# Optimization experiments

Measured on AMD Instinct MI355X. Metric: run time of the kernel, lower is better.

Reference implementation:

```python
import jax, jax.numpy as jnp
import numpy as np

NUM_HEADS = 16
EPS = 1e-5
BLOCK = 16  # score_mod: q_idx // 16 == kv_idx % 16


def _ln(x, eps=EPS):
    # LayerNorm, elementwise_affine=False
    m = jnp.mean(x, axis=-1, keepdims=True)
    v = jnp.mean((x - m) ** 2, axis=-1, keepdims=True)
    return (x - m) * jax.lax.rsqrt(v + eps)


def setup_inputs() -> dict:
    key = jax.random.key(0)
    ks = jax.random.split(key, 5)
    N, D = 2048, 2048
    w = 0.02
    return {
        "x": jax.random.normal(ks[0], (N, D), jnp.float32),
        "Wq": jax.random.normal(ks[1], (D, D), jnp.float32) * w,
        "Wk": jax.random.normal(ks[2], (D, D), jnp.float32) * w,
        "Wv": jax.random.normal(ks[3], (D, D), jnp.float32) * w,
        "Wo": jax.random.normal(ks[4], (D, D), jnp.float32) * w,
    }


def reference(x, Wq, Wk, Wv, Wo):
    N, D = x.shape
    H = NUM_HEADS
    DH = D // H
    x_in = x
    xn = _ln(x)
    # per-head q/k layernorm, cast to attention dtype (bfloat16)
    q = _ln((xn @ Wq).reshape(N, H, DH)).astype(jnp.bfloat16)
    k = _ln((xn @ Wk).reshape(N, H, DH)).astype(jnp.bfloat16)
    v = (xn @ Wv).reshape(N, H, DH)  # stays fp32 (original applies no cast to vs)
    scale = 1.0 / np.sqrt(DH)
    # dense scores then sparsity mask, as flex_attention with score_mod does
    scores = jnp.einsum("nhd,mhd->hnm", q, k, preferred_element_type=jnp.float32) * scale
    qi = jnp.arange(N)
    mask = (qi[:, None] // BLOCK) == (qi[None, :] % BLOCK)  # [N, N]
    s = jnp.where(mask[None, :, :], scores, -jnp.inf)
    # safe softmax: rows with no allowed keys (q_idx >= 256) produce zeros
    mx = jnp.max(s, axis=-1, keepdims=True)
    e = jnp.exp(s - jnp.where(jnp.isfinite(mx), mx, 0.0))
    denom = jnp.sum(e, axis=-1, keepdims=True)
    attn = e / jnp.maximum(denom, 1e-30)
    o = jnp.einsum("hnm,mhd->nhd", attn, v)  # [N, H, DH]
    out = o.reshape(N, D) @ Wo
    return out + x_in
```

## Files before the change

kernel.cpp:

```cpp
#include <hip/hip_runtime.h>

typedef unsigned short u16;
typedef __attribute__((ext_vector_type(8))) short short8;
typedef __attribute__((ext_vector_type(4))) float f32x4;

#define D 2048
#define EPS 1e-5f

__device__ __forceinline__ u16 f2bf(float f) {
  unsigned u = __float_as_uint(f);
  u += 0x7fffu + ((u >> 16) & 1u);
  return (u16)(u >> 16);
}

__device__ __forceinline__ void async16(const void* g, void* l) {
  __builtin_amdgcn_global_load_lds(
      (const __attribute__((address_space(1))) void*)g,
      (__attribute__((address_space(3))) void*)l, 16, 0, 0);
}

__global__ __launch_bounds__(256) void prep(const float* __restrict__ x,
                                            const float* __restrict__ Wq,
                                            const float* __restrict__ Wk,
                                            const float* __restrict__ Wv,
                                            const float* __restrict__ Wo,
                                            u16* __restrict__ xn,
                                            float* __restrict__ out,
                                            u16* __restrict__ WqT, u16* __restrict__ WkT,
                                            u16* __restrict__ WvT, u16* __restrict__ WoT) {
  int bid = blockIdx.x;
  int t = threadIdx.x;
  if (bid < 2048) {
    const float* xr = x + (size_t)bid * D;
    float4 v[2];
    float s = 0.f, sq = 0.f;
#pragma unroll
    for (int i = 0; i < 2; i++) {
      v[i] = *(const float4*)(xr + i * 1024 + t * 4);
      s += v[i].x + v[i].y + v[i].z + v[i].w;
      sq += v[i].x * v[i].x + v[i].y * v[i].y + v[i].z * v[i].z + v[i].w * v[i].w;
    }
#pragma unroll
    for (int m = 32; m >= 1; m >>= 1) { s += __shfl_xor(s, m); sq += __shfl_xor(sq, m); }
    __shared__ float ps[4], pq[4];
    int w = t >> 6, lane = t & 63;
    if (lane == 0) { ps[w] = s; pq[w] = sq; }
    __syncthreads();
    s = ps[0] + ps[1] + ps[2] + ps[3];
    sq = pq[0] + pq[1] + pq[2] + pq[3];
    float mean = s * (1.f / D);
    float var = sq * (1.f / D) - mean * mean;
    float rs = rsqrtf(var + EPS);
    float* outr = out + (size_t)bid * D;
    u16* xnr = xn + (size_t)bid * D;
#pragma unroll
    for (int i = 0; i < 2; i++) {
      *(float4*)(outr + i * 1024 + t * 4) = v[i];
      ushort4 o;
      o.x = f2bf((v[i].x - mean) * rs);
      o.y = f2bf((v[i].y - mean) * rs);
      o.z = f2bf((v[i].z - mean) * rs);
      o.w = f2bf((v[i].w - mean) * rs);
      *(ushort4*)(xnr + i * 1024 + t * 4) = o;
    }
  } else {
    int tb = bid - 2048;
    int wsel = tb >> 10;
    int tt = tb & 1023;
    const float* src; u16* dst;
    switch (wsel) {
      case 0: src = Wq; dst = WqT; break;
      case 1: src = Wk; dst = WkT; break;
      case 2: src = Wv; dst = WvT; break;
      default: src = Wo; dst = WoT; break;
    }
    int i0 = (tt >> 5) * 64, j0 = (tt & 31) * 64;
    __shared__ u16 tile[64 * 66];
#pragma unroll
    for (int r = 0; r < 4; r++) {
      int idx = r * 256 + t;
      int row = idx >> 4, c4 = idx & 15;
      float4 v = *(const float4*)(src + (size_t)(i0 + row) * D + j0 + c4 * 4);
      tile[row * 66 + c4 * 4 + 0] = f2bf(v.x);
      tile[row * 66 + c4 * 4 + 1] = f2bf(v.y);
      tile[row * 66 + c4 * 4 + 2] = f2bf(v.z);
      tile[row * 66 + c4 * 4 + 3] = f2bf(v.w);
    }
    __syncthreads();
#pragma unroll
    for (int r = 0; r < 4; r++) {
      int idx = r * 256 + t;
      int row = idx >> 4, c4 = idx & 15;
      ushort4 o;
      o.x = tile[(c4 * 4 + 0) * 66 + row];
      o.y = tile[(c4 * 4 + 1) * 66 + row];
      o.z = tile[(c4 * 4 + 2) * 66 + row];
      o.w = tile[(c4 * 4 + 3) * 66 + row];
      *(ushort4*)(dst + (size_t)(j0 + row) * D + i0 + c4 * 4) = o;
    }
  }
}

__device__ __forceinline__ void gemm_tile(const u16* __restrict__ A,
                                          const u16* __restrict__ Bt,
                                          bool permB, int m0, int n0,
                                          int kbeg, int kend,
                                          u16* As, u16* Bs, f32x4 acc[4][4]) {
  int tid = threadIdx.x, wid = tid >> 6, lane = tid & 63;
  int q4 = lane >> 4, m16 = lane & 15;
  int wm = wid >> 1, wn = wid & 1;
  for (int kb = kbeg; kb < kend; kb += 64) {
#pragma unroll
    for (int p = 0; p < 4; p++) {
      int idx = p * 256 + tid;
      int r = idx >> 3, sl = idx & 7;
      int gc = sl ^ (r & 7);
      async16(A + (size_t)(m0 + r) * D + kb + gc * 8, As + (size_t)(p * 256 + wid * 64) * 8);
      int rb = n0 + r;
      int gr = permB ? ((rb & 127) * 16 + (rb >> 7)) : rb;
      async16(Bt + (size_t)gr * D + kb + gc * 8, Bs + (size_t)(p * 256 + wid * 64) * 8);
    }
    __syncthreads();
#pragma unroll
    for (int ks = 0; ks < 2; ks++) {
      short8 af[4], bf[4];
      int c = ks * 4 + q4;
#pragma unroll
      for (int i = 0; i < 4; i++) {
        int ra = wm * 64 + i * 16 + m16;
        af[i] = *(const short8*)(As + ra * 64 + (c ^ (ra & 7)) * 8);
        int rb = wn * 64 + i * 16 + m16;
        bf[i] = *(const short8*)(Bs + rb * 64 + (c ^ (rb & 7)) * 8);
      }
#pragma unroll
      for (int i = 0; i < 4; i++)
#pragma unroll
        for (int j = 0; j < 4; j++)
          acc[i][j] = __builtin_amdgcn_mfma_f32_16x16x32_bf16(af[i], bf[j], acc[i][j], 0, 0, 0);
    }
    __syncthreads();
  }
}

__global__ __launch_bounds__(256, 3) void gemm_mega(const u16* __restrict__ xn,
                                                    const u16* __restrict__ WkT,
                                                    const u16* __restrict__ WqT,
                                                    const u16* __restrict__ WvT,
                                                    u16* __restrict__ K3,
                                                    u16* __restrict__ Q3,
                                                    u16* __restrict__ V3) {
  __shared__ u16 smem[2 * 128 * 64];
  u16* As = smem;
  u16* Bs = smem + 8192;
  int bid = blockIdx.x;
  int sel = (bid < 256) ? 0 : (bid < 512) ? 2 : 1;
  int z = (sel == 1) ? bid - 512 : (bid & 255);
  int m0 = (z >> 4) * 128, n0 = (z & 15) * 128;
  const u16* A = (sel == 2) ? WvT : xn;
  const u16* Bt = (sel == 0) ? WkT : (sel == 1) ? WqT : xn;
  f32x4 acc[4][4];
#pragma unroll
  for (int i = 0; i < 4; i++)
#pragma unroll
    for (int j = 0; j < 4; j++)
#pragma unroll
      for (int r = 0; r < 4; r++) acc[i][j][r] = 0.f;
  gemm_tile(A, Bt, sel == 2, m0, n0, 0, D, As, Bs, acc);

  int tid = threadIdx.x, wid = tid >> 6, lane = tid & 63;
  int q4 = lane >> 4, m16 = lane & 15;
  int wm = wid >> 1, wn = wid & 1;
  if (sel == 2) {
    int h = m0 >> 7, b = n0 >> 7;
#pragma unroll
    for (int i = 0; i < 4; i++)
#pragma unroll
      for (int j = 0; j < 4; j++)
#pragma unroll
        for (int r = 0; r < 4; r++) {
          int dhl = wm * 64 + i * 16 + q4 * 4 + r;
          int key = wn * 64 + j * 16 + m16;
          V3[((size_t)(h * 16 + b) * 128 + dhl) * 128 + key] = f2bf(acc[i][j][r]);
        }
  } else {
    float* redS = (float*)smem;
    float* redQ = redS + 256;
    __syncthreads();
#pragma unroll
    for (int i = 0; i < 4; i++) {
      float ps[4], pq[4];
#pragma unroll
      for (int r = 0; r < 4; r++) {
        float s = 0.f, q = 0.f;
#pragma unroll
        for (int j = 0; j < 4; j++) { float a = acc[i][j][r]; s += a; q += a * a; }
#pragma unroll
        for (int msk = 1; msk < 16; msk <<= 1) {
          s += __shfl_xor(s, msk);
          q += __shfl_xor(q, msk);
        }
        ps[r] = s; pq[r] = q;
      }
      if (m16 == 0) {
#pragma unroll
        for (int r = 0; r < 4; r++) {
          int row = wm * 64 + i * 16 + q4 * 4 + r;
          redS[row * 2 + wn] = ps[r];
          redQ[row * 2 + wn] = pq[r];
        }
      }
    }
    __syncthreads();
    int h = n0 >> 7;
#pragma unroll
    for (int i = 0; i < 4; i++)
#pragma unroll
      for (int r = 0; r < 4; r++) {
        int row = wm * 64 + i * 16 + q4 * 4 + r;
        float S = redS[row * 2] + redS[row * 2 + 1];
        float Qs = redQ[row * 2] + redQ[row * 2 + 1];
        float mean = S * (1.f / 128.f);
        float var = Qs * (1.f / 128.f) - mean * mean;
        float rstd = rsqrtf(var + EPS);
        int tok = m0 + row;
#pragma unroll
        for (int j = 0; j < 4; j++) {
          int dhl = wn * 64 + j * 16 + m16;
          u16 val = f2bf((acc[i][j][r] - mean) * rstd);
          if (sel == 0)
            K3[(((size_t)(h * 16 + (tok & 15))) * 128 + (tok >> 4)) * 128 + dhl] = val;
          else
            Q3[((size_t)h * 256 + tok) * 128 + dhl] = val;
        }
      }
  }
}

__global__ __launch_bounds__(128) void attn(const u16* __restrict__ Q3,
                                            const u16* __restrict__ K3,
                                            const u16* __restrict__ V3,
                                            u16* __restrict__ Ob) {
  int bh = blockIdx.x;
  int b = bh & 15, h = bh >> 4;
  int tid = threadIdx.x, w = tid >> 6, lane = tid & 63;
  int q4 = lane >> 4, m16 = lane & 15;
  __shared__ float redmx[2][16];
  __shared__ float redsm[2][16];
  __shared__ float invd[16];
  __shared__ u16 P[16][136];
  const float scale = 0.08838834764831845f;
  const u16* Ktile = K3 + (size_t)(h * 16 + b) * 128 * 128;
  const u16* Vtile = V3 + (size_t)(h * 16 + b) * 128 * 128;

  short8 af[4];
#pragma unroll
  for (int dc = 0; dc < 4; dc++)
    af[dc] = *(const short8*)(Q3 + ((size_t)h * 256 + b * 16 + m16) * 128 + dc * 32 + q4 * 8);
  f32x4 s[4];
#pragma unroll
  for (int kt = 0; kt < 4; kt++)
#pragma unroll
    for (int r = 0; r < 4; r++) s[kt][r] = 0.f;
#pragma unroll
  for (int kt = 0; kt < 4; kt++) {
    int key = w * 64 + kt * 16 + m16;
#pragma unroll
    for (int dc = 0; dc < 4; dc++) {
      short8 bf = *(const short8*)(Ktile + (size_t)key * 128 + dc * 32 + q4 * 8);
      s[kt] = __builtin_amdgcn_mfma_f32_16x16x32_bf16(af[dc], bf, s[kt], 0, 0, 0);
    }
  }
  float mx[4];
#pragma unroll
  for (int r = 0; r < 4; r++) {
    mx[r] = fmaxf(fmaxf(s[0][r], s[1][r]), fmaxf(s[2][r], s[3][r]));
#pragma unroll
    for (int msk = 1; msk < 16; msk <<= 1) mx[r] = fmaxf(mx[r], __shfl_xor(mx[r], msk));
  }
  if (m16 == 0) {
#pragma unroll
    for (int r = 0; r < 4; r++) redmx[w][q4 * 4 + r] = mx[r];
  }
  __syncthreads();
#pragma unroll
  for (int r = 0; r < 4; r++) {
    float M = fmaxf(redmx[0][q4 * 4 + r], redmx[1][q4 * 4 + r]);
    float acc = 0.f;
#pragma unroll
    for (int kt = 0; kt < 4; kt++) {
      float e = __expf((s[kt][r] - M) * scale);
      s[kt][r] = e;
      acc += e;
    }
#pragma unroll
    for (int msk = 1; msk < 16; msk <<= 1) acc += __shfl_xor(acc, msk);
    if (m16 == 0) redsm[w][q4 * 4 + r] = acc;
  }
#pragma unroll
  for (int kt = 0; kt < 4; kt++)
#pragma unroll
    for (int r = 0; r < 4; r++)
      P[q4 * 4 + r][w * 64 + kt * 16 + m16] = f2bf(s[kt][r]);
  __syncthreads();
  if (tid < 16) invd[tid] = 1.0f / (redsm[0][tid] + redsm[1][tid]);
  __syncthreads();

  short8 pf[4];
#pragma unroll
  for (int kc = 0; kc < 4; kc++)
    pf[kc] = *(const short8*)(&P[m16][kc * 32 + q4 * 8]);
  f32x4 o[4];
#pragma unroll
  for (int dt = 0; dt < 4; dt++)
#pragma unroll
    for (int r = 0; r < 4; r++) o[dt][r] = 0.f;
#pragma unroll
  for (int dt = 0; dt < 4; dt++) {
    int dhl = (w * 4 + dt) * 16 + m16;
#pragma unroll
    for (int kc = 0; kc < 4; kc++) {
      short8 vf = *(const short8*)(Vtile + (size_t)dhl * 128 + kc * 32 + q4 * 8);
      o[dt] = __builtin_amdgcn_mfma_f32_16x16x32_bf16(pf[kc], vf, o[dt], 0, 0, 0);
    }
  }
#pragma unroll
  for (int dt = 0; dt < 4; dt++)
#pragma unroll
    for (int r = 0; r < 4; r++) {
      int row = q4 * 4 + r;
      float val = o[dt][r] * invd[row];
      Ob[(size_t)(b * 16 + row) * D + h * 128 + (w * 4 + dt) * 16 + m16] = f2bf(val);
    }
}

__global__ __launch_bounds__(256, 3) void gemm_wo(const u16* __restrict__ Ob,
                                                  const u16* __restrict__ WoT,
                                                  float* __restrict__ Wpart) {
  __shared__ u16 smem[2 * 128 * 64];
  u16* As = smem;
  u16* Bs = smem + 8192;
  int m0 = blockIdx.x * 128, n0 = blockIdx.y * 128;
  int z = blockIdx.z;
  int k0 = z * 256;
  f32x4 acc[4][4];
#pragma unroll
  for (int i = 0; i < 4; i++)
#pragma unroll
    for (int j = 0; j < 4; j++)
#pragma unroll
      for (int r = 0; r < 4; r++) acc[i][j][r] = 0.f;
  gemm_tile(Ob, WoT, false, m0, n0, k0, k0 + 256, As, Bs, acc);
  float* C = Wpart + (size_t)z * 256 * D;
  int tid = threadIdx.x, wid = tid >> 6, lane = tid & 63;
  int q4 = lane >> 4, m16 = lane & 15;
  int wm = wid >> 1, wn = wid & 1;
#pragma unroll
  for (int i = 0; i < 4; i++)
#pragma unroll
    for (int j = 0; j < 4; j++)
#pragma unroll
      for (int r = 0; r < 4; r++) {
        int row = m0 + wm * 64 + i * 16 + q4 * 4 + r;
        int col = n0 + wn * 64 + j * 16 + m16;
        C[(size_t)row * D + col] = acc[i][j][r];
      }
}

__global__ __launch_bounds__(256) void reduce_wo(const float* __restrict__ Wpart,
                                                 float* __restrict__ out) {
  int i = (blockIdx.x * 256 + threadIdx.x) * 4;
  float4 s = *(const float4*)(out + i);
#pragma unroll
  for (int z = 0; z < 8; z++) {
    float4 p = *(const float4*)(Wpart + (size_t)z * 256 * D + i);
    s.x += p.x; s.y += p.y; s.z += p.z; s.w += p.w;
  }
  *(float4*)(out + i) = s;
}

extern "C" void kernel_launch(void* const* d_in, const int* in_sizes, int n_in,
                              void* d_out, int out_size, void* d_ws, size_t ws_size,
                              hipStream_t stream) {
  const float* x  = (const float*)d_in[0];
  const float* Wq = (const float*)d_in[1];
  const float* Wk = (const float*)d_in[2];
  const float* Wv = (const float*)d_in[3];
  const float* Wo = (const float*)d_in[4];
  float* out = (float*)d_out;
  char* w = (char*)d_ws;
  const size_t MB = 1u << 20;
  u16*   xn    = (u16*)(w);
  u16*   WqT   = (u16*)(w + 8 * MB);
  u16*   WkT   = (u16*)(w + 16 * MB);
  u16*   WvT   = (u16*)(w + 24 * MB);
  u16*   WoT   = (u16*)(w + 32 * MB);
  u16*   K3    = (u16*)(w + 40 * MB);
  u16*   V3    = (u16*)(w + 48 * MB);
  u16*   Q3    = (u16*)(w + 56 * MB);
  u16*   Obf   = (u16*)(w + 57 * MB);
  float* Wpart = (float*)(w + 58 * MB);

  prep<<<dim3(6144), dim3(256), 0, stream>>>(x, Wq, Wk, Wv, Wo, xn, out, WqT, WkT, WvT, WoT);
  gemm_mega<<<dim3(544), dim3(256), 0, stream>>>(xn, WkT, WqT, WvT, K3, Q3, V3);
  attn<<<dim3(256), dim3(128), 0, stream>>>(Q3, K3, V3, Obf);
  gemm_wo<<<dim3(2, 16, 8), dim3(256), 0, stream>>>(Obf, WoT, Wpart);
  reduce_wo<<<dim3(512), dim3(256), 0, stream>>>(Wpart, out);
}
```

Measured before the change: 195.3 us.

## Fuse Q projection into attention kernel and replace Wo split-K reduce with atomics

Removes the Q projection tiles from the mega GEMM and computes Q (plus per-head layernorm) inside each attention block directly from xn and WqT with MFMA, writing it to shared memory. The attention block grows to 4 waves, each handling 32 keys or head dims. The separate reduce kernel for the split-K Wo GEMM is dropped in favour of float atomic adds into the output, which is pre-initialised with the residual. This saves a kernel launch and the Q3/Wpart round trips. The cost is that the Q GEMM reads its operands straight from global memory without LDS tiling, and atomics make the summation order non-deterministic.

```diff
diff --git a/kernel.cpp b/kernel.cpp
--- a/kernel.cpp
+++ b/kernel.cpp
@@ -144,20 +144,18 @@
 
 __global__ __launch_bounds__(256, 3) void gemm_mega(const u16* __restrict__ xn,
                                                     const u16* __restrict__ WkT,
-                                                    const u16* __restrict__ WqT,
                                                     const u16* __restrict__ WvT,
                                                     u16* __restrict__ K3,
-                                                    u16* __restrict__ Q3,
                                                     u16* __restrict__ V3) {
   __shared__ u16 smem[2 * 128 * 64];
   u16* As = smem;
   u16* Bs = smem + 8192;
   int bid = blockIdx.x;
-  int sel = (bid < 256) ? 0 : (bid < 512) ? 2 : 1;
-  int z = (sel == 1) ? bid - 512 : (bid & 255);
+  int sel = bid >> 8;
+  int z = bid & 255;
   int m0 = (z >> 4) * 128, n0 = (z & 15) * 128;
-  const u16* A = (sel == 2) ? WvT : xn;
-  const u16* Bt = (sel == 0) ? WkT : (sel == 1) ? WqT : xn;
+  const u16* A = sel ? WvT : xn;
+  const u16* Bt = sel ? xn : WkT;
   f32x4 acc[4][4];
 #pragma unroll
   for (int i = 0; i < 4; i++)
@@ -165,12 +163,12 @@
     for (int j = 0; j < 4; j++)
 #pragma unroll
       for (int r = 0; r < 4; r++) acc[i][j][r] = 0.f;
-  gemm_tile(A, Bt, sel == 2, m0, n0, 0, D, As, Bs, acc);
+  gemm_tile(A, Bt, sel == 1, m0, n0, 0, D, As, Bs, acc);
 
   int tid = threadIdx.x, wid = tid >> 6, lane = tid & 63;
   int q4 = lane >> 4, m16 = lane & 15;
   int wm = wid >> 1, wn = wid & 1;
-  if (sel == 2) {
+  if (sel == 1) {
     int h = m0 >> 7, b = n0 >> 7;
 #pragma unroll
     for (int i = 0; i < 4; i++)
@@ -227,43 +225,82 @@
         for (int j = 0; j < 4; j++) {
           int dhl = wn * 64 + j * 16 + m16;
           u16 val = f2bf((acc[i][j][r] - mean) * rstd);
-          if (sel == 0)
-            K3[(((size_t)(h * 16 + (tok & 15))) * 128 + (tok >> 4)) * 128 + dhl] = val;
-          else
-            Q3[((size_t)h * 256 + tok) * 128 + dhl] = val;
+          K3[(((size_t)(h * 16 + (tok & 15))) * 128 + (tok >> 4)) * 128 + dhl] = val;
         }
       }
   }
 }
 
-__global__ __launch_bounds__(128) void attn(const u16* __restrict__ Q3,
+__global__ __launch_bounds__(256) void attn(const u16* __restrict__ xn,
+                                            const u16* __restrict__ WqT,
                                             const u16* __restrict__ K3,
                                             const u16* __restrict__ V3,
                                             u16* __restrict__ Ob) {
   int bh = blockIdx.x;
-  int b = bh & 15, h = bh >> 4;
+  int h = bh & 15, b = bh >> 4;
   int tid = threadIdx.x, w = tid >> 6, lane = tid & 63;
   int q4 = lane >> 4, m16 = lane & 15;
-  __shared__ float redmx[2][16];
-  __shared__ float redsm[2][16];
+  __shared__ u16 Qs[16][136];
+  __shared__ u16 P[16][136];
+  __shared__ float redA[16][4];
+  __shared__ float redB[16][4];
+  __shared__ float redmx[4][16];
+  __shared__ float redsm[4][16];
   __shared__ float invd[16];
-  __shared__ u16 P[16][136];
   const float scale = 0.08838834764831845f;
   const u16* Ktile = K3 + (size_t)(h * 16 + b) * 128 * 128;
   const u16* Vtile = V3 + (size_t)(h * 16 + b) * 128 * 128;
 
+  f32x4 qa[2];
+#pragma unroll
+  for (int nt = 0; nt < 2; nt++)
+#pragma unroll
+    for (int r = 0; r < 4; r++) qa[nt][r] = 0.f;
+  const u16* xr = xn + (size_t)(b * 16 + m16) * D + q4 * 8;
+  const u16* wr = WqT + (size_t)(h * 128 + w * 32 + m16) * D + q4 * 8;
+#pragma unroll 4
+  for (int kk = 0; kk < D; kk += 32) {
+    short8 a = *(const short8*)(xr + kk);
+    short8 b0 = *(const short8*)(wr + kk);
+    short8 b1 = *(const short8*)(wr + 16 * D + kk);
+    qa[0] = __builtin_amdgcn_mfma_f32_16x16x32_bf16(a, b0, qa[0], 0, 0, 0);
+    qa[1] = __builtin_amdgcn_mfma_f32_16x16x32_bf16(a, b1, qa[1], 0, 0, 0);
+  }
+#pragma unroll
+  for (int r = 0; r < 4; r++) {
+    float s = qa[0][r] + qa[1][r];
+    float q2 = qa[0][r] * qa[0][r] + qa[1][r] * qa[1][r];
+#pragma unroll
+    for (int msk = 1; msk < 16; msk <<= 1) { s += __shfl_xor(s, msk); q2 += __shfl_xor(q2, msk); }
+    if (m16 == 0) { redA[q4 * 4 + r][w] = s; redB[q4 * 4 + r][w] = q2; }
+  }
+  __syncthreads();
+#pragma unroll
+  for (int r = 0; r < 4; r++) {
+    int row = q4 * 4 + r;
+    float S = redA[row][0] + redA[row][1] + redA[row][2] + redA[row][3];
+    float Q2 = redB[row][0] + redB[row][1] + redB[row][2] + redB[row][3];
+    float mean = S * (1.f / 128.f);
+    float var = Q2 * (1.f / 128.f) - mean * mean;
+    float rstd = rsqrtf(var + EPS);
+#pragma unroll
+    for (int nt = 0; nt < 2; nt++)
+      Qs[row][w * 32 + nt * 16 + m16] = f2bf((qa[nt][r] - mean) * rstd);
+  }
+  __syncthreads();
+
   short8 af[4];
 #pragma unroll
   for (int dc = 0; dc < 4; dc++)
-    af[dc] = *(const short8*)(Q3 + ((size_t)h * 256 + b * 16 + m16) * 128 + dc * 32 + q4 * 8);
-  f32x4 s[4];
-#pragma unroll
-  for (int kt = 0; kt < 4; kt++)
+    af[dc] = *(const short8*)(&Qs[m16][dc * 32 + q4 * 8]);
+  f32x4 s[2];
+#pragma unroll
+  for (int kt = 0; kt < 2; kt++)
 #pragma unroll
     for (int r = 0; r < 4; r++) s[kt][r] = 0.f;
 #pragma unroll
-  for (int kt = 0; kt < 4; kt++) {
-    int key = w * 64 + kt * 16 + m16;
+  for (int kt = 0; kt < 2; kt++) {
+    int key = w * 32 + kt * 16 + m16;
 #pragma unroll
     for (int dc = 0; dc < 4; dc++) {
       short8 bf = *(const short8*)(Ktile + (size_t)key * 128 + dc * 32 + q4 * 8);
@@ -273,50 +310,48 @@
   float mx[4];
 #pragma unroll
   for (int r = 0; r < 4; r++) {
-    mx[r] = fmaxf(fmaxf(s[0][r], s[1][r]), fmaxf(s[2][r], s[3][r]));
+    mx[r] = fmaxf(s[0][r], s[1][r]);
 #pragma unroll
     for (int msk = 1; msk < 16; msk <<= 1) mx[r] = fmaxf(mx[r], __shfl_xor(mx[r], msk));
-  }
-  if (m16 == 0) {
-#pragma unroll
-    for (int r = 0; r < 4; r++) redmx[w][q4 * 4 + r] = mx[r];
+    if (m16 == 0) redmx[w][q4 * 4 + r] = mx[r];
   }
   __syncthreads();
 #pragma unroll
   for (int r = 0; r < 4; r++) {
-    float M = fmaxf(redmx[0][q4 * 4 + r], redmx[1][q4 * 4 + r]);
+    int row = q4 * 4 + r;
+    float M = fmaxf(fmaxf(redmx[0][row], redmx[1][row]), fmaxf(redmx[2][row], redmx[3][row]));
     float acc = 0.f;
 #pragma unroll
-    for (int kt = 0; kt < 4; kt++) {
+    for (int kt = 0; kt < 2; kt++) {
       float e = __expf((s[kt][r] - M) * scale);
       s[kt][r] = e;
       acc += e;
     }
 #pragma unroll
     for (int msk = 1; msk < 16; msk <<= 1) acc += __shfl_xor(acc, msk);
-    if (m16 == 0) redsm[w][q4 * 4 + r] = acc;
-  }
-#pragma unroll
-  for (int kt = 0; kt < 4; kt++)
+    if (m16 == 0) redsm[w][row] = acc;
+  }
+#pragma unroll
+  for (int kt = 0; kt < 2; kt++)
 #pragma unroll
     for (int r = 0; r < 4; r++)
-      P[q4 * 4 + r][w * 64 + kt * 16 + m16] = f2bf(s[kt][r]);
+      P[q4 * 4 + r][w * 32 + kt * 16 + m16] = f2bf(s[kt][r]);
   __syncthreads();
-  if (tid < 16) invd[tid] = 1.0f / (redsm[0][tid] + redsm[1][tid]);
+  if (tid < 16) invd[tid] = 1.0f / (redsm[0][tid] + redsm[1][tid] + redsm[2][tid] + redsm[3][tid]);
   __syncthreads();
 
   short8 pf[4];
 #pragma unroll
   for (int kc = 0; kc < 4; kc++)
     pf[kc] = *(const short8*)(&P[m16][kc * 32 + q4 * 8]);
-  f32x4 o[4];
-#pragma unroll
-  for (int dt = 0; dt < 4; dt++)
+  f32x4 o[2];
+#pragma unroll
+  for (int dt = 0; dt < 2; dt++)
 #pragma unroll
     for (int r = 0; r < 4; r++) o[dt][r] = 0.f;
 #pragma unroll
-  for (int dt = 0; dt < 4; dt++) {
-    int dhl = (w * 4 + dt) * 16 + m16;
+  for (int dt = 0; dt < 2; dt++) {
+    int dhl = w * 32 + dt * 16 + m16;
 #pragma unroll
     for (int kc = 0; kc < 4; kc++) {
       short8 vf = *(const short8*)(Vtile + (size_t)dhl * 128 + kc * 32 + q4 * 8);
@@ -324,18 +359,18 @@
     }
   }
 #pragma unroll
-  for (int dt = 0; dt < 4; dt++)
+  for (int dt = 0; dt < 2; dt++)
 #pragma unroll
     for (int r = 0; r < 4; r++) {
       int row = q4 * 4 + r;
       float val = o[dt][r] * invd[row];
-      Ob[(size_t)(b * 16 + row) * D + h * 128 + (w * 4 + dt) * 16 + m16] = f2bf(val);
+      Ob[(size_t)(b * 16 + row) * D + h * 128 + w * 32 + dt * 16 + m16] = f2bf(val);
     }
 }
 
 __global__ __launch_bounds__(256, 3) void gemm_wo(const u16* __restrict__ Ob,
                                                   const u16* __restrict__ WoT,
-                                                  float* __restrict__ Wpart) {
+                                                  float* __restrict__ out) {
   __shared__ u16 smem[2 * 128 * 64];
   u16* As = smem;
   u16* Bs = smem + 8192;
@@ -350,7 +385,6 @@
 #pragma unroll
       for (int r = 0; r < 4; r++) acc[i][j][r] = 0.f;
   gemm_tile(Ob, WoT, false, m0, n0, k0, k0 + 256, As, Bs, acc);
-  float* C = Wpart + (size_t)z * 256 * D;
   int tid = threadIdx.x, wid = tid >> 6, lane = tid & 63;
   int q4 = lane >> 4, m16 = lane & 15;
   int wm = wid >> 1, wn = wid & 1;
@@ -362,20 +396,8 @@
       for (int r = 0; r < 4; r++) {
         int row = m0 + wm * 64 + i * 16 + q4 * 4 + r;
         int col = n0 + wn * 64 + j * 16 + m16;
-        C[(size_t)row * D + col] = acc[i][j][r];
+        unsafeAtomicAdd(&out[(size_t)row * D + col], acc[i][j][r]);
       }
-}
-
-__global__ __launch_bounds__(256) void reduce_wo(const float* __restrict__ Wpart,
-                                                 float* __restrict__ out) {
-  int i = (blockIdx.x * 256 + threadIdx.x) * 4;
-  float4 s = *(const float4*)(out + i);
-#pragma unroll
-  for (int z = 0; z < 8; z++) {
-    float4 p = *(const float4*)(Wpart + (size_t)z * 256 * D + i);
-    s.x += p.x; s.y += p.y; s.z += p.z; s.w += p.w;
-  }
-  *(float4*)(out + i) = s;
 }
 
 extern "C" void kernel_launch(void* const* d_in, const int* in_sizes, int n_in,
@@ -396,13 +418,10 @@
   u16*   WoT   = (u16*)(w + 32 * MB);
   u16*   K3    = (u16*)(w + 40 * MB);
   u16*   V3    = (u16*)(w + 48 * MB);
-  u16*   Q3    = (u16*)(w + 56 * MB);
-  u16*   Obf   = (u16*)(w + 57 * MB);
-  float* Wpart = (float*)(w + 58 * MB);
+  u16*   Obf   = (u16*)(w + 56 * MB);
 
   prep<<<dim3(6144), dim3(256), 0, stream>>>(x, Wq, Wk, Wv, Wo, xn, out, WqT, WkT, WvT, WoT);
-  gemm_mega<<<dim3(544), dim3(256), 0, stream>>>(xn, WkT, WqT, WvT, K3, Q3, V3);
-  attn<<<dim3(256), dim3(128), 0, stream>>>(Q3, K3, V3, Obf);
-  gemm_wo<<<dim3(2, 16, 8), dim3(256), 0, stream>>>(Obf, WoT, Wpart);
-  reduce_wo<<<dim3(512), dim3(256), 0, stream>>>(Wpart, out);
-}
+  gemm_mega<<<dim3(512), dim3(256), 0, stream>>>(xn, WkT, WvT, K3, V3);
+  attn<<<dim3(256), dim3(256), 0, stream>>>(xn, WqT, K3, V3, Obf);
+  gemm_wo<<<dim3(2, 16, 8), dim3(256), 0, stream>>>(Obf, WoT, out);
+}
```

New measurement: 215.0 us. 10.1% more time.
